# Performance work log

Measured on AMD Instinct MI355X. Metric: run time of the kernel, lower is better.

Reference implementation:

```python
import jax, jax.numpy as jnp
import numpy as np

N = 100000   # nodes
E = 3200000  # directed edges
F = 16       # num_features (colors)


def setup_inputs() -> dict:
    key = jax.random.key(0)
    ks = jax.random.split(key, 5)
    x = jax.random.normal(ks[0], (N, F), dtype=jnp.float32)
    edge_index = jax.random.randint(ks[1], (2, E), 0, N)
    # Glorot-ish scaled weights for the 5 identical blocks (F->64->32->F)
    W1 = jax.random.normal(ks[2], (5, F, 64), dtype=jnp.float32) * (1.0 / np.sqrt(F))
    W2 = jax.random.normal(ks[3], (5, 64, 32), dtype=jnp.float32) * (1.0 / np.sqrt(64))
    W3 = jax.random.normal(ks[4], (5, 32, F), dtype=jnp.float32) * (1.0 / np.sqrt(32))
    b1 = jnp.zeros((5, 64), dtype=jnp.float32)
    b2 = jnp.zeros((5, 32), dtype=jnp.float32)
    b3 = jnp.zeros((5, F), dtype=jnp.float32)
    return {"x": x, "edge_index": edge_index,
            "W1": W1, "b1": b1, "W2": W2, "b2": b2, "W3": W3, "b3": b3}


def _gcn(x, W, b, src, dst, norm, n):
    # GCNConv: project, then symmetric-normalized neighbor sum (self-loops in src/dst)
    h = x @ W                                   # [n, d_out]
    msg = h[src] * norm[:, None]                # [e+n, d_out] gather + scale
    out = jax.ops.segment_sum(msg, dst, num_segments=n)
    return out + b


def reference(x, edge_index, W1, b1, W2, b2, W3, b3):
    n = x.shape[0]
    loops = jnp.arange(n)
    src = jnp.concatenate([edge_index[0], loops])  # add self loops (PyG default)
    dst = jnp.concatenate([edge_index[1], loops])
    deg = jax.ops.segment_sum(jnp.ones(src.shape[0], jnp.float32), dst, num_segments=n)
    dis = jax.lax.rsqrt(jnp.maximum(deg, 1.0))     # deg >= 1 due to self loops
    norm = dis[src] * dis[dst]
    for i in range(5):
        x = jax.nn.relu(_gcn(x, W1[i], b1[i], src, dst, norm, n))
        x = jax.nn.relu(_gcn(x, W2[i], b2[i], src, dst, norm, n))
        x = jax.nn.softmax(_gcn(x, W3[i], b3[i], src, dst, norm, n), axis=1)
    return x
```

## Files before the change

kernel.cpp:

```cpp
#include <hip/hip_runtime.h>

#define NN 100000
#define NE 3200000
#define SLAB 80
#define SLAB4 (SLAB / 4)
#define NB 196
#define BSH 9
#define BCAP 20480
#define NBB 1024
#define EPB 3125

typedef int      vi4 __attribute__((ext_vector_type(4)));
typedef float    vf4 __attribute__((ext_vector_type(4)));
typedef _Float16 vh8 __attribute__((ext_vector_type(8)));


__global__ __launch_bounds__(256)
void k_bucket(const int* __restrict__ src, const int* __restrict__ dst,
              int* __restrict__ gcur, int* __restrict__ entries) {
    __shared__ int scnt[NB];
    __shared__ int sofs[NB];
    __shared__ int sbase[NB];
    __shared__ int sfill[NB];
    __shared__ int tmp[256];
    __shared__ int stage[EPB];
    int tid = threadIdx.x;
    for (int i = tid; i < NB; i += 256) { scnt[i] = 0; sfill[i] = 0; }
    __syncthreads();
    int e0 = blockIdx.x * EPB;
    int e1 = e0 + EPB;
    for (int e = e0 + tid; e < e1; e += 256)
        atomicAdd(&scnt[__builtin_nontemporal_load(dst + e) >> BSH], 1);
    __syncthreads();
    tmp[tid] = (tid < NB) ? scnt[tid] : 0;
    __syncthreads();
    #pragma unroll
    for (int o = 1; o < 256; o <<= 1) {
        int v = (tid >= o) ? tmp[tid - o] : 0;
        __syncthreads();
        tmp[tid] += v;
        __syncthreads();
    }
    if (tid < NB) {
        sofs[tid] = tmp[tid] - scnt[tid];
        sbase[tid] = atomicAdd(&gcur[tid], scnt[tid]);
    }
    __syncthreads();
    for (int e = e0 + tid; e < e1; e += 256) {
        int d = __builtin_nontemporal_load(dst + e);
        int s = __builtin_nontemporal_load(src + e);
        int b = d >> BSH;
        int pos = sofs[b] + atomicAdd(&sfill[b], 1);
        stage[pos] = s | ((d & 511) << 17);
    }
    __syncthreads();
    int wid = tid >> 6, lane = tid & 63;
    for (int b = wid; b < NB; b += 4) {
        int cnt = scnt[b];
        int gbase = sbase[b];
        int lbase = sofs[b];
        for (int j = lane; j < cnt; j += 64) {
            int pos = gbase + j;
            if (pos < BCAP)
                __builtin_nontemporal_store(stage[lbase + j], entries + b * BCAP + pos);
        }
    }
}

__global__ __launch_bounds__(512)
void k_csr(const int* __restrict__ gcur, const int* __restrict__ entries,
           int* __restrict__ col, int* __restrict__ cnt4, float* __restrict__ dis,
           const float* __restrict__ x, vh8* __restrict__ xs8,
           vh8* __restrict__ h3s8, vh8* __restrict__ h2s8) {
    __shared__ int lcur[512];
    int tid = threadIdx.x;
    int b = blockIdx.x;
    lcur[tid] = 0;
    __syncthreads();
    int nE = min(gcur[b], BCAP);
    const int* ep = entries + b * BCAP;
    int nbase = b << BSH;
    for (int e = tid; e < nE; e += 512) {
        int v = __builtin_nontemporal_load(ep + e);
        int s = v & 0x1FFFF;
        int local = v >> 17;
        int p = atomicAdd(&lcur[local], 1);
        if (p < SLAB) col[(size_t)(nbase + local) * SLAB + p] = s;
    }
    __syncthreads();
    {
        int node = nbase + tid;
        if (node < NN) {
            int c = lcur[tid];
            float dn = rsqrtf((float)(c + 1));
            dis[node] = dn;
            int cc = min(c, SLAB);
            int c4 = (cc + 3) >> 2;
            cnt4[node] = c4;
            int* slab = col + (size_t)node * SLAB;
            for (int k = cc; k < c4 * 4; k++) slab[k] = NN;
            const vf4* xr = (const vf4*)(x + (size_t)node * 16);
            vh8 o0, o1;
            #pragma unroll
            for (int i = 0; i < 4; i++) {
                o0[i]     = (_Float16)(xr[0][i] * dn);
                o0[i + 4] = (_Float16)(xr[1][i] * dn);
                o1[i]     = (_Float16)(xr[2][i] * dn);
                o1[i + 4] = (_Float16)(xr[3][i] * dn);
            }
            xs8[(size_t)node * 2 + 0] = o0;
            xs8[(size_t)node * 2 + 1] = o1;
        }
    }
    if (b == 0 && tid < 8) {
        vh8 z = {(_Float16)0.f, (_Float16)0.f, (_Float16)0.f, (_Float16)0.f,
                 (_Float16)0.f, (_Float16)0.f, (_Float16)0.f, (_Float16)0.f};
        if (tid < 2)      xs8[NN * 2 + tid] = z;
        else if (tid < 4) h3s8[NN * 2 + (tid - 2)] = z;
        else              h2s8[NN * 4 + (tid - 4)] = z;
    }
}

template<int CH, int UNROLL>
__device__ inline void gather4w(const vh8* __restrict__ in, const int4* __restrict__ cp,
                                int c4, int node, int d, int h, float* acc) {
    vh8 self = in[node * CH + d];
    #pragma unroll
    for (int i = 0; i < 8; i++) acc[i] = h ? 0.f : (float)self[i];
    #pragma unroll UNROLL
    for (int k = h; k < c4; k += 4) {
        vi4 cs = __builtin_nontemporal_load((const vi4*)(cp + k));
        vh8 a = in[cs.x * CH + d];
        vh8 b = in[cs.y * CH + d];
        vh8 c = in[cs.z * CH + d];
        vh8 e = in[cs.w * CH + d];
        #pragma unroll
        for (int i = 0; i < 8; i++)
            acc[i] += ((float)a[i] + (float)b[i]) + ((float)c[i] + (float)e[i]);
    }
    #pragma unroll
    for (int i = 0; i < 8; i++) acc[i] += __shfl_xor(acc[i], 1);
    #pragma unroll
    for (int i = 0; i < 8; i++) acc[i] += __shfl_xor(acc[i], 2);
}


__global__ __launch_bounds__(256)
void k_layerA(const vh8* __restrict__ xs, const int* __restrict__ cnt4,
              const int4* __restrict__ colv, const float* __restrict__ dis,
              const float* __restrict__ W1, const float* __restrict__ b1,
              const float* __restrict__ W2, _Float16* __restrict__ h2s) {
    __shared__ float sW1[16 * 64];
    __shared__ float sW2[64 * 32];
    __shared__ float sb1[64];
    __shared__ float st[32 * 16];
    __shared__ _Float16 sx1h[32 * 72];
    int tid = threadIdx.x;
    for (int i = tid; i < 16 * 64; i += 256) sW1[i] = W1[i];
    for (int i = tid; i < 64 * 32; i += 256) sW2[i] = W2[i];
    if (tid < 64) sb1[tid] = b1[tid];

    int nl = tid >> 3, ll = tid & 7, d = ll >> 2, h = ll & 3;
    int node = blockIdx.x * 32 + nl;
    float dn = dis[node];
    float acc[8];
    gather4w<2, 2>(xs, colv + (size_t)node * SLAB4, cnt4[node], node, d, h, acc);
    if (h == 0) {
        vf4 v0 = {acc[0] * dn, acc[1] * dn, acc[2] * dn, acc[3] * dn};
        vf4 v1 = {acc[4] * dn, acc[5] * dn, acc[6] * dn, acc[7] * dn};
        ((vf4*)st)[nl * 4 + d * 2 + 0] = v0;
        ((vf4*)st)[nl * 4 + d * 2 + 1] = v1;
    }
    __syncthreads();

    int c = tid & 63, g = tid >> 6;
    #pragma unroll
    for (int p = 0; p < 2; p++) {
        int nb = g * 8 + p * 4;
        float a0 = sb1[c], a1 = a0, a2 = a0, a3 = a0;
        #pragma unroll
        for (int k = 0; k < 16; k++) {
            float w = sW1[k * 64 + c];
            a0 += st[(nb + 0) * 16 + k] * w;
            a1 += st[(nb + 1) * 16 + k] * w;
            a2 += st[(nb + 2) * 16 + k] * w;
            a3 += st[(nb + 3) * 16 + k] * w;
        }
        sx1h[(nb + 0) * 72 + c] = (_Float16)fmaxf(a0, 0.f);
        sx1h[(nb + 1) * 72 + c] = (_Float16)fmaxf(a1, 0.f);
        sx1h[(nb + 2) * 72 + c] = (_Float16)fmaxf(a2, 0.f);
        sx1h[(nb + 3) * 72 + c] = (_Float16)fmaxf(a3, 0.f);
    }
    __syncthreads();

    int c2 = tid & 31, g2 = tid >> 5;
    #pragma unroll
    for (int p = 0; p < 4; p++) {
        int n2 = g2 * 4 + p;
        const vh8* xr = (const vh8*)(sx1h + n2 * 72);
        float a = 0.f;
        #pragma unroll
        for (int j = 0; j < 8; j++) {
            vh8 v = xr[j];
            #pragma unroll
            for (int i = 0; i < 8; i++)
                a += (float)v[i] * sW2[(j * 8 + i) * 32 + c2];
        }
        int gn = blockIdx.x * 32 + n2;
        h2s[(size_t)gn * 32 + c2] = (_Float16)(a * dis[gn]);
    }
}

__global__ __launch_bounds__(256)
void k_aggmm3(const vh8* __restrict__ h2s, const int* __restrict__ cnt4,
              const int4* __restrict__ colv, const float* __restrict__ dis,
              const float* __restrict__ b2, const float* __restrict__ W3,
              _Float16* __restrict__ h3s) {
    __shared__ float sW[32 * 16];
    __shared__ float sb[32];
    __shared__ float st[16 * 40];
    int tid = threadIdx.x;
    for (int i = tid; i < 32 * 16; i += 256) sW[i] = W3[i];
    if (tid < 32) sb[tid] = b2[tid];
    __syncthreads();

    int nl = tid >> 4, ll = tid & 15, d = ll >> 2, h = ll & 3;
    int node = blockIdx.x * 16 + nl;
    float dn = dis[node];
    float acc[8];
    gather4w<4, 2>(h2s, colv + (size_t)node * SLAB4, cnt4[node], node, d, h, acc);
    if (h == 0) {
        vf4 v0, v1;
        #pragma unroll
        for (int i = 0; i < 4; i++) {
            v0[i] = fmaxf(acc[i] * dn + sb[d * 8 + i], 0.f);
            v1[i] = fmaxf(acc[i + 4] * dn + sb[d * 8 + 4 + i], 0.f);
        }
        vf4* sp = (vf4*)(st + nl * 40 + d * 8);
        sp[0] = v0;
        sp[1] = v1;
    }
    __syncthreads();

    int c = tid & 15, n = tid >> 4;
    float a0 = 0.f;
    #pragma unroll
    for (int k = 0; k < 32; k++) a0 += st[n * 40 + k] * sW[k * 16 + c];
    int gn = blockIdx.x * 16 + n;
    h3s[(size_t)gn * 16 + c] = (_Float16)(a0 * dis[gn]);
}

__global__ __launch_bounds__(256)
void k_agg_soft(const vh8* __restrict__ in, const int* __restrict__ cnt4,
                const int4* __restrict__ colv, const float* __restrict__ dis,
                const float* __restrict__ bias, float* __restrict__ out,
                vh8* __restrict__ out2) {
    int tid = threadIdx.x;
    int nl = tid >> 3, ll = tid & 7, d = ll >> 2, h = ll & 3;
    int node = blockIdx.x * 32 + nl;
    float dn = dis[node];
    float acc[8];
    gather4w<2, 2>(in, colv + (size_t)node * SLAB4, cnt4[node], node, d, h, acc);
    #pragma unroll
    for (int i = 0; i < 8; i++) acc[i] = acc[i] * dn + bias[d * 8 + i];
    float m = acc[0];
    #pragma unroll
    for (int i = 1; i < 8; i++) m = fmaxf(m, acc[i]);
    m = fmaxf(m, __shfl_xor(m, 4));
    float ev[8], s = 0.f;
    #pragma unroll
    for (int i = 0; i < 8; i++) { ev[i] = __expf(acc[i] - m); s += ev[i]; }
    s += __shfl_xor(s, 4);
    float inv = 1.0f / s;
    if (h == 0) {
        vf4 o0 = {ev[0] * inv, ev[1] * inv, ev[2] * inv, ev[3] * inv};
        vf4 o1 = {ev[4] * inv, ev[5] * inv, ev[6] * inv, ev[7] * inv};
        __builtin_nontemporal_store(o0, (vf4*)out + (size_t)node * 4 + d * 2);
        __builtin_nontemporal_store(o1, (vf4*)out + (size_t)node * 4 + d * 2 + 1);
        vh8 ho;
        #pragma unroll
        for (int i = 0; i < 8; i++) ho[i] = (_Float16)(ev[i] * inv * dn);
        out2[(size_t)node * 2 + d] = ho;
    }
}


static inline size_t align_up(size_t v, size_t a) { return (v + a - 1) & ~(a - 1); }

extern "C" void kernel_launch(void* const* d_in, const int* in_sizes, int n_in,
                              void* d_out, int out_size, void* d_ws, size_t ws_size,
                              hipStream_t stream) {
    const float* x   = (const float*)d_in[0];
    const int*   ei  = (const int*)d_in[1];
    const float* W1  = (const float*)d_in[2];
    const float* b1  = (const float*)d_in[3];
    const float* W2  = (const float*)d_in[4];
    const float* b2  = (const float*)d_in[5];
    const float* W3  = (const float*)d_in[6];
    const float* b3  = (const float*)d_in[7];
    float* outp = (float*)d_out;

    const int* src = ei;
    const int* dst = ei + NE;

    char* ws = (char*)d_ws;
    size_t off = 0;
    auto carve = [&](size_t bytes) { void* p = ws + off; off = align_up(off + bytes, 256); return p; };
    int*      gcur  = (int*)     carve(NB * 4);
    int*      cnt4  = (int*)     carve(NN * 4);
    float*    dis   = (float*)   carve(NN * 4);
    int*      col   = (int*)     carve((size_t)NN * SLAB * 4);
    _Float16* xs    = (_Float16*)carve((size_t)(NN + 1) * 16 * 2);
    _Float16* h3s   = (_Float16*)carve((size_t)(NN + 1) * 16 * 2);
    int*      entries = (int*)   carve((size_t)NB * BCAP * 4);
    _Float16* h2s   = (_Float16*)carve((size_t)(NN + 1) * 32 * 2);
    (void)ws_size; (void)n_in; (void)in_sizes; (void)out_size;

    hipMemsetAsync(gcur, 0, NB * 4, stream);
    k_bucket<<<NBB, 256, 0, stream>>>(src, dst, gcur, entries);
    k_csr<<<NB, 512, 0, stream>>>(gcur, entries, col, cnt4, dis, x,
                                  (vh8*)xs, (vh8*)h3s, (vh8*)h2s);

    const int gA = NN / 32;
    const int gB = NN / 16;
    const int gC = NN / 32;

    for (int l = 0; l < 5; l++) {
        k_layerA<<<gA, 256, 0, stream>>>((const vh8*)xs, cnt4, (const int4*)col, dis,
                                         W1 + l * 16 * 64, b1 + l * 64, W2 + l * 64 * 32, h2s);
        k_aggmm3<<<gB, 256, 0, stream>>>((const vh8*)h2s, cnt4, (const int4*)col, dis,
                                         b2 + l * 32, W3 + l * 32 * 16, h3s);
        k_agg_soft<<<gC, 256, 0, stream>>>((const vh8*)h3s, cnt4, (const int4*)col, dis,
                                           b3 + l * 16, outp, (vh8*)xs);
    }
}
```

Before: 705.3 us.

## Sort nodes by degree bucket to balance gather work within wavefronts

Adds a degree histogram in the CSR build and a counting-sort kernel that orders node ids by padded neighbor-count. All aggregation kernels then process nodes in that sorted order, so the 4-lane groups in a wavefront have similar loop trip counts and less divergence. The cost is an extra kernel, a sorted-id indirection, and scattered row writes and self/col reads that lose the spatial locality of sequential node order. NBIN=21 assumes c4 never exceeds 20, which holds because SLAB=80.

```diff
diff --git a/kernel.cpp b/kernel.cpp
--- a/kernel.cpp
+++ b/kernel.cpp
@@ -9,6 +9,7 @@
 #define BCAP 20480
 #define NBB 1024
 #define EPB 3125
+#define NBIN 21
 
 typedef int      vi4 __attribute__((ext_vector_type(4)));
 typedef float    vf4 __attribute__((ext_vector_type(4)));
@@ -71,7 +72,8 @@
 void k_csr(const int* __restrict__ gcur, const int* __restrict__ entries,
            int* __restrict__ col, int* __restrict__ cnt4, float* __restrict__ dis,
            const float* __restrict__ x, vh8* __restrict__ xs8,
-           vh8* __restrict__ h3s8, vh8* __restrict__ h2s8) {
+           vh8* __restrict__ h3s8, vh8* __restrict__ h2s8,
+           int* __restrict__ hist) {
     __shared__ int lcur[512];
     int tid = threadIdx.x;
     int b = blockIdx.x;
@@ -97,6 +99,7 @@
             int cc = min(c, SLAB);
             int c4 = (cc + 3) >> 2;
             cnt4[node] = c4;
+            atomicAdd(&hist[c4], 1);
             int* slab = col + (size_t)node * SLAB;
             for (int k = cc; k < c4 * 4; k++) slab[k] = NN;
             const vf4* xr = (const vf4*)(x + (size_t)node * 16);
@@ -121,6 +124,31 @@
     }
 }
 
+__global__ __launch_bounds__(256)
+void k_sort(const int* __restrict__ cnt4, const int* __restrict__ hist,
+            int* __restrict__ doff, int* __restrict__ sorted_ids) {
+    __shared__ int lh[NBIN];
+    __shared__ int lbase[NBIN];
+    int tid = threadIdx.x;
+    if (tid < NBIN) lh[tid] = 0;
+    __syncthreads();
+    int i = blockIdx.x * 256 + tid;
+    int c4 = 0, lpos = 0;
+    if (i < NN) {
+        c4 = cnt4[i];
+        lpos = atomicAdd(&lh[c4], 1);
+    }
+    __syncthreads();
+    if (tid < NBIN && lh[tid] > 0)
+        lbase[tid] = atomicAdd(&doff[tid], lh[tid]);
+    __syncthreads();
+    if (i < NN) {
+        int base = 0;
+        for (int j = 0; j < c4; j++) base += hist[j];
+        sorted_ids[base + lbase[c4] + lpos] = i;
+    }
+}
+
 template<int CH, int UNROLL>
 __device__ inline void gather4w(const vh8* __restrict__ in, const int4* __restrict__ cp,
                                 int c4, int node, int d, int h, float* acc) {
@@ -148,6 +176,7 @@
 __global__ __launch_bounds__(256)
 void k_layerA(const vh8* __restrict__ xs, const int* __restrict__ cnt4,
               const int4* __restrict__ colv, const float* __restrict__ dis,
+              const int* __restrict__ sid,
               const float* __restrict__ W1, const float* __restrict__ b1,
               const float* __restrict__ W2, _Float16* __restrict__ h2s) {
     __shared__ float sW1[16 * 64];
@@ -155,13 +184,16 @@
     __shared__ float sb1[64];
     __shared__ float st[32 * 16];
     __shared__ _Float16 sx1h[32 * 72];
+    __shared__ int sids[32];
     int tid = threadIdx.x;
     for (int i = tid; i < 16 * 64; i += 256) sW1[i] = W1[i];
     for (int i = tid; i < 64 * 32; i += 256) sW2[i] = W2[i];
     if (tid < 64) sb1[tid] = b1[tid];
+    if (tid < 32) sids[tid] = sid[blockIdx.x * 32 + tid];
+    __syncthreads();
 
     int nl = tid >> 3, ll = tid & 7, d = ll >> 2, h = ll & 3;
-    int node = blockIdx.x * 32 + nl;
+    int node = sids[nl];
     float dn = dis[node];
     float acc[8];
     gather4w<2, 2>(xs, colv + (size_t)node * SLAB4, cnt4[node], node, d, h, acc);
@@ -206,7 +238,7 @@
             for (int i = 0; i < 8; i++)
                 a += (float)v[i] * sW2[(j * 8 + i) * 32 + c2];
         }
-        int gn = blockIdx.x * 32 + n2;
+        int gn = sids[n2];
         h2s[(size_t)gn * 32 + c2] = (_Float16)(a * dis[gn]);
     }
 }
@@ -214,18 +246,21 @@
 __global__ __launch_bounds__(256)
 void k_aggmm3(const vh8* __restrict__ h2s, const int* __restrict__ cnt4,
               const int4* __restrict__ colv, const float* __restrict__ dis,
+              const int* __restrict__ sid,
               const float* __restrict__ b2, const float* __restrict__ W3,
               _Float16* __restrict__ h3s) {
     __shared__ float sW[32 * 16];
     __shared__ float sb[32];
     __shared__ float st[16 * 40];
+    __shared__ int sids[16];
     int tid = threadIdx.x;
     for (int i = tid; i < 32 * 16; i += 256) sW[i] = W3[i];
     if (tid < 32) sb[tid] = b2[tid];
+    if (tid < 16) sids[tid] = sid[blockIdx.x * 16 + tid];
     __syncthreads();
 
     int nl = tid >> 4, ll = tid & 15, d = ll >> 2, h = ll & 3;
-    int node = blockIdx.x * 16 + nl;
+    int node = sids[nl];
     float dn = dis[node];
     float acc[8];
     gather4w<4, 2>(h2s, colv + (size_t)node * SLAB4, cnt4[node], node, d, h, acc);
@@ -246,18 +281,19 @@
     float a0 = 0.f;
     #pragma unroll
     for (int k = 0; k < 32; k++) a0 += st[n * 40 + k] * sW[k * 16 + c];
-    int gn = blockIdx.x * 16 + n;
+    int gn = sids[n];
     h3s[(size_t)gn * 16 + c] = (_Float16)(a0 * dis[gn]);
 }
 
 __global__ __launch_bounds__(256)
 void k_agg_soft(const vh8* __restrict__ in, const int* __restrict__ cnt4,
                 const int4* __restrict__ colv, const float* __restrict__ dis,
+                const int* __restrict__ sid,
                 const float* __restrict__ bias, float* __restrict__ out,
                 vh8* __restrict__ out2) {
     int tid = threadIdx.x;
     int nl = tid >> 3, ll = tid & 7, d = ll >> 2, h = ll & 3;
-    int node = blockIdx.x * 32 + nl;
+    int node = sid[blockIdx.x * 32 + nl];
     float dn = dis[node];
     float acc[8];
     gather4w<2, 2>(in, colv + (size_t)node * SLAB4, cnt4[node], node, d, h, acc);
@@ -306,9 +342,13 @@
     char* ws = (char*)d_ws;
     size_t off = 0;
     auto carve = [&](size_t bytes) { void* p = ws + off; off = align_up(off + bytes, 256); return p; };
-    int*      gcur  = (int*)     carve(NB * 4);
+    int*      meta  = (int*)     carve((NB + 64) * 4);
+    int*      gcur  = meta;
+    int*      hist  = meta + NB;
+    int*      doff  = meta + NB + 32;
     int*      cnt4  = (int*)     carve(NN * 4);
     float*    dis   = (float*)   carve(NN * 4);
+    int*      sids  = (int*)     carve(NN * 4);
     int*      col   = (int*)     carve((size_t)NN * SLAB * 4);
     _Float16* xs    = (_Float16*)carve((size_t)(NN + 1) * 16 * 2);
     _Float16* h3s   = (_Float16*)carve((size_t)(NN + 1) * 16 * 2);
@@ -316,21 +356,22 @@
     _Float16* h2s   = (_Float16*)carve((size_t)(NN + 1) * 32 * 2);
     (void)ws_size; (void)n_in; (void)in_sizes; (void)out_size;
 
-    hipMemsetAsync(gcur, 0, NB * 4, stream);
+    hipMemsetAsync(meta, 0, (NB + 64) * 4, stream);
     k_bucket<<<NBB, 256, 0, stream>>>(src, dst, gcur, entries);
     k_csr<<<NB, 512, 0, stream>>>(gcur, entries, col, cnt4, dis, x,
-                                  (vh8*)xs, (vh8*)h3s, (vh8*)h2s);
+                                  (vh8*)xs, (vh8*)h3s, (vh8*)h2s, hist);
+    k_sort<<<(NN + 255) / 256, 256, 0, stream>>>(cnt4, hist, doff, sids);
 
     const int gA = NN / 32;
     const int gB = NN / 16;
     const int gC = NN / 32;
 
     for (int l = 0; l < 5; l++) {
-        k_layerA<<<gA, 256, 0, stream>>>((const vh8*)xs, cnt4, (const int4*)col, dis,
+        k_layerA<<<gA, 256, 0, stream>>>((const vh8*)xs, cnt4, (const int4*)col, dis, sids,
                                          W1 + l * 16 * 64, b1 + l * 64, W2 + l * 64 * 32, h2s);
-        k_aggmm3<<<gB, 256, 0, stream>>>((const vh8*)h2s, cnt4, (const int4*)col, dis,
+        k_aggmm3<<<gB, 256, 0, stream>>>((const vh8*)h2s, cnt4, (const int4*)col, dis, sids,
                                          b2 + l * 32, W3 + l * 32 * 16, h3s);
-        k_agg_soft<<<gC, 256, 0, stream>>>((const vh8*)h3s, cnt4, (const int4*)col, dis,
+        k_agg_soft<<<gC, 256, 0, stream>>>((const vh8*)h3s, cnt4, (const int4*)col, dis, sids,
                                            b3 + l * 16, outp, (vh8*)xs);
     }
 }
```

New measurement: 1.237 ms. 1.75x slower.
